# Kernel optimization log

Hardware: AMD Instinct MI355X
Metric: run time of the kernel (lower is better)

Reference implementation:

```python
import jax, jax.numpy as jnp
import numpy as np

WIDTH = 2048
NUM_HEADS = 16
HEAD_DIM = WIDTH // NUM_HEADS  # 128
ROPE_DIMS = HEAD_DIM // 2      # 64, partial rotary
WINDOW = 512
ROPE_BASE = 10000.0
NEG_INF = -1e9


def apply_rope(x, dims, offset=0, base=ROPE_BASE):
    # x: [B, H, L, hd]; non-traditional (half-split) rotary on first `dims` dims.
    L = x.shape[2]
    half = dims // 2
    pos = (offset + jnp.arange(L)).astype(x.dtype)                     # [L]
    inv_freq = jnp.exp(-jnp.log(jnp.asarray(base, x.dtype)) * (jnp.arange(0, dims, 2).astype(x.dtype) / dims))  # [half]
    theta = pos[:, None] * inv_freq[None, :]                           # [L, half]
    cos = jnp.cos(theta)[None, None]                                   # [1,1,L,half]
    sin = jnp.sin(theta)[None, None]
    x1 = x[..., :half]
    x2 = x[..., half:dims]
    rest = x[..., dims:]
    rx1 = x1 * cos - x2 * sin
    rx2 = x1 * sin + x2 * cos
    return jnp.concatenate([rx1, rx2, rest], axis=-1)


def setup_inputs() -> dict:
    key = jax.random.key(0)
    ks = jax.random.split(key, 6)
    B, L, D, hd = 2, 2048, WIDTH, HEAD_DIM
    x = jax.random.normal(ks[0], (B, L, D), dtype=jnp.float32)
    Wq = jax.random.normal(ks[1], (D, D), dtype=jnp.float32) * 0.02
    Wk = jax.random.normal(ks[2], (D, hd), dtype=jnp.float32) * 0.02
    Wv = jax.random.normal(ks[3], (D, hd), dtype=jnp.float32) * 0.02
    Wo = jax.random.normal(ks[4], (D, D), dtype=jnp.float32) * 0.02
    bo = jax.random.normal(ks[5], (D,), dtype=jnp.float32) * 0.02
    return {"x": x, "Wq": Wq, "Wk": Wk, "Wv": Wv, "Wo": Wo, "bo": bo}


def reference(x, Wq, Wk, Wv, Wo, bo):
    B, L, D = x.shape
    H, hd = NUM_HEADS, HEAD_DIM
    scale = hd ** (-0.5)

    q = (x @ Wq).reshape(B, L, H, hd).transpose(0, 2, 1, 3)   # [B,H,L,hd]
    k = (x @ Wk).reshape(B, L, 1, hd).transpose(0, 2, 1, 3)   # [B,1,L,hd] (MQA)
    v = (x @ Wv).reshape(B, L, 1, hd).transpose(0, 2, 1, 3)

    q = apply_rope(q, ROPE_DIMS)
    k = apply_rope(k, ROPE_DIMS)

    # sliding-window causal mask: attend iff 0 <= i - j < WINDOW
    i = jnp.arange(L)[:, None]
    j = jnp.arange(L)[None, :]
    allowed = (i - j >= 0) & (i - j < WINDOW)                  # [L,L]
    mask = jnp.where(allowed, 0.0, NEG_INF).astype(x.dtype)

    scores = jnp.einsum("bhqd,bkd->bhqk", q, k[:, 0]) * scale  # [B,H,L,L]
    scores = scores + mask[None, None]
    attn = jax.nn.softmax(scores, axis=-1)
    out = jnp.einsum("bhqk,bkd->bhqd", attn, v[:, 0])          # [B,H,L,hd]
    out = out.transpose(0, 2, 1, 3).reshape(B, L, D)
    return out @ Wo + bo
```

## Files before the change

### kernel.cpp

```cpp
#include <hip/hip_runtime.h>
#include <hip/hip_bf16.h>
#include <stdint.h>


typedef float  f32x4  __attribute__((ext_vector_type(4)));
typedef __bf16 bf16x8 __attribute__((ext_vector_type(8)));

#define ASYNC_LD16(gp, lp)                                                     \
  __builtin_amdgcn_global_load_lds(                                            \
      (__attribute__((address_space(1))) void*)(gp),                           \
      (__attribute__((address_space(3))) void*)(lp), 16, 0, 0)

__global__ __launch_bounds__(256) void prep_all(
    const float* __restrict__ x, __hip_bfloat16* __restrict__ xb,
    const float* __restrict__ Wq, const float* __restrict__ Wk,
    const float* __restrict__ Wv, const float* __restrict__ Wo,
    __hip_bfloat16* __restrict__ wqkvT, __hip_bfloat16* __restrict__ woT) {
  __shared__ float t[32][33];
  int bid = blockIdx.x;
  if (bid < 8192) {
    const int i = bid * 256 + threadIdx.x;
    const float4 v = ((const float4*)x)[i];
    __align__(8) __hip_bfloat16 o[4] = {
        __float2bfloat16(v.x), __float2bfloat16(v.y),
        __float2bfloat16(v.z), __float2bfloat16(v.w)};
    *(uint2*)(xb + (size_t)i * 4) = *(uint2*)o;
    return;
  }
  bid -= 8192;
  const float* src;
  __hip_bfloat16* dst;
  int C, cb, rb;
  if (bid < 4096) {
    src = Wq; dst = wqkvT; C = 2048; cb = bid & 63; rb = bid >> 6;
  } else if (bid < 4352) {
    const int l = bid - 4096;
    src = Wk; dst = wqkvT + 2048ull * 2048; C = 128; cb = l & 3; rb = l >> 2;
  } else if (bid < 4608) {
    const int l = bid - 4352;
    src = Wv; dst = wqkvT + 2176ull * 2048; C = 128; cb = l & 3; rb = l >> 2;
  } else {
    const int l = bid - 4608;
    src = Wo; dst = woT; C = 2048; cb = l & 63; rb = l >> 6;
  }
  const int c0 = cb * 32, r0 = rb * 32;
  const int xx = threadIdx.x & 31, y = threadIdx.x >> 5;
#pragma unroll
  for (int i = 0; i < 32; i += 8)
    t[y + i][xx] = src[(size_t)(r0 + y + i) * C + c0 + xx];
  __syncthreads();
#pragma unroll
  for (int i = 0; i < 32; i += 8)
    dst[(size_t)(c0 + y + i) * 2048 + r0 + xx] = __float2bfloat16(t[xx][y + i]);
}

__device__ __forceinline__ void gemm_core64(const __bf16* __restrict__ A,
                                            const __bf16* __restrict__ BT,
                                            int K, __bf16* As, __bf16* Bs,
                                            f32x4 (&acc)[4][4]) {
  const int tid = threadIdx.x;
  const int wave = tid >> 6;
  const int lane = tid & 63;
  const int m0 = blockIdx.y * 128;
  const int n0 = blockIdx.x * 128;
  const int wm = (wave & 1) * 64;
  const int wn = (wave >> 1) * 64;
  const int ln = lane & 15;
  const int quad = lane >> 4;
  const int rdoff = (quad ^ ((ln >> 1) & 3)) * 8;

  size_t goff[4];
  int ldsoff[4];
#pragma unroll
  for (int i = 0; i < 4; i++) {
    const int cidx = (wave * 4 + i) * 64 + lane;
    const int p = cidx >> 9;
    const int pidx = cidx & 511;
    const int row = pidx >> 2;
    const int cc = pidx & 3;
    const int cg = cc ^ ((row >> 1) & 3);
    goff[i] = (size_t)row * K + p * 32 + cg * 8;
    ldsoff[i] = (wave * 4 + i) * 512;
  }
  const __bf16* Abase = A + (size_t)m0 * K;
  const __bf16* Bbase = BT + (size_t)n0 * K;

  for (int k0 = 0; k0 < K; k0 += 64) {
#pragma unroll
    for (int i = 0; i < 4; i++)
      ASYNC_LD16(Abase + k0 + goff[i], As + ldsoff[i]);
#pragma unroll
    for (int i = 0; i < 4; i++)
      ASYNC_LD16(Bbase + k0 + goff[i], Bs + ldsoff[i]);
    __syncthreads();
    bf16x8 af[4][2], bf[4][2];
#pragma unroll
    for (int i = 0; i < 4; i++)
#pragma unroll
      for (int p = 0; p < 2; p++)
        af[i][p] = *(const bf16x8*)&As[p * 4096 + (wm + i * 16 + ln) * 32 + rdoff];
#pragma unroll
    for (int j = 0; j < 4; j++)
#pragma unroll
      for (int p = 0; p < 2; p++)
        bf[j][p] = *(const bf16x8*)&Bs[p * 4096 + (wn + j * 16 + ln) * 32 + rdoff];
#pragma unroll
    for (int p = 0; p < 2; p++)
#pragma unroll
      for (int i = 0; i < 4; i++)
#pragma unroll
        for (int j = 0; j < 4; j++)
          acc[i][j] = __builtin_amdgcn_mfma_f32_16x16x32_bf16(af[i][p], bf[j][p],
                                                              acc[i][j], 0, 0, 0);
    __syncthreads();
  }
}

__global__ __launch_bounds__(256) void gemm_qkv(
    const __bf16* __restrict__ A, const __bf16* __restrict__ BT,
    __hip_bfloat16* __restrict__ qd, __hip_bfloat16* __restrict__ kd,
    __hip_bfloat16* __restrict__ vtd, int K) {
  __shared__ __align__(16) __bf16 As[128 * 64];
  __shared__ __align__(16) __bf16 Bs[128 * 64];
  f32x4 acc[4][4];
  const f32x4 zero = {0.f, 0.f, 0.f, 0.f};
#pragma unroll
  for (int i = 0; i < 4; i++)
#pragma unroll
    for (int j = 0; j < 4; j++) acc[i][j] = zero;
  gemm_core64(A, BT, K, As, Bs, acc);

  const int tid = threadIdx.x;
  const int wave = tid >> 6;
  const int lane = tid & 63;
  const int quad = lane >> 4;
  const int ln = lane & 15;
  const int m0 = blockIdx.y * 128;
  const int n0 = blockIdx.x * 128;
  const int wm = (wave & 1) * 64;
  const int wn = (wave >> 1) * 64;

  if (n0 == 2176) {
    const int bb = m0 >> 11;
    const int mloc = m0 & 2047;
#pragma unroll
    for (int i = 0; i < 4; i++) {
      const int rb = mloc + wm + i * 16 + quad * 4;
#pragma unroll
      for (int j = 0; j < 4; j++) {
        const int col = wn + j * 16 + ln;
        __align__(8) __hip_bfloat16 t4[4];
#pragma unroll
        for (int r = 0; r < 4; r++) t4[r] = __float2bfloat16(acc[i][j][r]);
        *(uint2*)(vtd + ((size_t)(bb * 128 + col)) * 2048 + rb) = *(uint2*)t4;
      }
    }
    return;
  }

  __hip_bfloat16* dst;
  int dstride, dcol;
  if (n0 < 2048) {
    dst = qd; dstride = 2048; dcol = n0;
  } else {
    dst = kd; dstride = 128; dcol = 0;
  }
  const bool dorope = (wn == 0);
  float invf0 = 0.f, invf1 = 0.f;
  if (dorope) {
    invf0 = expf(-0.28782313662425574f * (float)ln);
    invf1 = expf(-0.28782313662425574f * (float)(16 + ln));
  }

#pragma unroll
  for (int i = 0; i < 4; i++) {
#pragma unroll
    for (int r = 0; r < 4; r++) {
      const int row = m0 + wm + i * 16 + quad * 4 + r;
      float o0 = acc[i][0][r], o1 = acc[i][1][r];
      float o2 = acc[i][2][r], o3 = acc[i][3][r];
      if (dorope) {
        const float pos = (float)(row & 2047);
        float s0, c0, s1, c1;
        __sincosf(pos * invf0, &s0, &c0);
        __sincosf(pos * invf1, &s1, &c1);
        const float a0 = o0, b0 = o2, a1 = o1, b1 = o3;
        o0 = a0 * c0 - b0 * s0;
        o2 = a0 * s0 + b0 * c0;
        o1 = a1 * c1 - b1 * s1;
        o3 = a1 * s1 + b1 * c1;
      }
      __hip_bfloat16* rp = dst + (size_t)row * dstride + dcol + wn + ln;
      rp[0]  = __float2bfloat16(o0);
      rp[16] = __float2bfloat16(o1);
      rp[32] = __float2bfloat16(o2);
      rp[48] = __float2bfloat16(o3);
    }
  }
}

__global__ __launch_bounds__(256) void gemm_out(
    const __bf16* __restrict__ A, const __bf16* __restrict__ BT,
    float* __restrict__ C, const float* __restrict__ bias, int N, int K) {
  __shared__ __align__(16) __bf16 As[128 * 64];
  __shared__ __align__(16) __bf16 Bs[128 * 64];
  f32x4 acc[4][4];
  const f32x4 zero = {0.f, 0.f, 0.f, 0.f};
#pragma unroll
  for (int i = 0; i < 4; i++)
#pragma unroll
    for (int j = 0; j < 4; j++) acc[i][j] = zero;
  gemm_core64(A, BT, K, As, Bs, acc);

  const int tid = threadIdx.x;
  const int wave = tid >> 6;
  const int lane = tid & 63;
  const int m0 = blockIdx.y * 128;
  const int n0 = blockIdx.x * 128;
  const int wm = (wave & 1) * 64;
  const int wn = (wave >> 1) * 64;
  const int lrow = lane & 15;
#pragma unroll
  for (int j = 0; j < 4; j++) {
    const int col = n0 + wn + j * 16 + lrow;
    const float bv = bias[col];
#pragma unroll
    for (int i = 0; i < 4; i++) {
#pragma unroll
      for (int r = 0; r < 4; r++) {
        const int row = m0 + wm + i * 16 + (lane >> 4) * 4 + r;
        C[(size_t)row * N + col] = acc[i][j][r] + bv;
      }
    }
  }
}

__global__ __launch_bounds__(256) void attn_mfma(
    const __bf16* __restrict__ qb,
    const __bf16* __restrict__ kb,
    const __bf16* __restrict__ vtb,
    __hip_bfloat16* __restrict__ o)
{
  __shared__ __align__(16) __bf16 Ks[4][64 * 32];
  __shared__ __align__(16) __bf16 Vs[2][128 * 32];
  __shared__ __align__(16) __bf16 Ps[4][2][2][512];
  const int tid = threadIdx.x;
  const int wave = tid >> 6;
  const int lane = tid & 63;
  const int quad = lane >> 4;
  const int ln = lane & 15;
  const int bid = blockIdx.x;
  const int q0 = (bid & 15) * 128;
  const int h = (bid >> 4) & 15;
  const int b = bid >> 8;
  const int swr = (ln >> 1) & 3;
  const int rdoff = (quad ^ swr) * 8;

  bf16x8 qf[2][4];
#pragma unroll
  for (int g = 0; g < 2; g++) {
    const __bf16* qrow =
        qb + ((size_t)(b * 2048 + q0 + wave * 32 + g * 16 + ln)) * 2048 + h * 128;
#pragma unroll
    for (int ks = 0; ks < 4; ks++)
      qf[g][ks] = *(const bf16x8*)(qrow + ks * 32 + quad * 8);
  }

  f32x4 oacc[2][8];
  const f32x4 zero = {0.f, 0.f, 0.f, 0.f};
#pragma unroll
  for (int g = 0; g < 2; g++)
#pragma unroll
    for (int nb = 0; nb < 8; nb++) oacc[g][nb] = zero;
  float li[2][4] = {{0.f, 0.f, 0.f, 0.f}, {0.f, 0.f, 0.f, 0.f}};
  const float scale = 0.08838834764831845f;

  const __bf16* kbase = kb + (size_t)b * 2048 * 128;
  const __bf16* vbase = vtb + (size_t)b * 128 * 2048;

  const int tstart = (q0 >= 512) ? 0 : (512 - q0) / 64;
  for (int t = tstart; t < 10; ++t) {
    const int jt = q0 - 512 + 64 * t;
    __syncthreads();
    {
      const int key4 = lane >> 2, uu = lane & 3;
      const int sw = (key4 >> 1) & 3;
#pragma unroll
      for (int i = 0; i < 4; ++i) {
        const int c = wave * 4 + i;
        const int ks = c & 3, keybase = (c >> 2) * 16;
        ASYNC_LD16(kbase + (size_t)(jt + keybase + key4) * 128 + ks * 32 +
                       (uu ^ sw) * 8,
                   &Ks[ks][keybase * 32]);
      }
#pragma unroll
      for (int i = 0; i < 4; ++i) {
        const int c = wave * 4 + i;
        const int p = c & 1, dbase = (c >> 1) * 16;
        ASYNC_LD16(vbase + (size_t)(dbase + key4) * 2048 + jt + p * 32 +
                       (uu ^ sw) * 8,
                   &Vs[p][dbase * 32]);
      }
    }
    __syncthreads();

    f32x4 sacc[2][4];
#pragma unroll
    for (int g = 0; g < 2; g++)
#pragma unroll
      for (int j = 0; j < 4; j++) sacc[g][j] = zero;
#pragma unroll
    for (int j = 0; j < 4; j++)
#pragma unroll
      for (int ks = 0; ks < 4; ks++) {
        const bf16x8 kf = *(const bf16x8*)&Ks[ks][(j * 16 + ln) * 32 + rdoff];
#pragma unroll
        for (int g = 0; g < 2; g++)
          sacc[g][j] = __builtin_amdgcn_mfma_f32_16x16x32_bf16(qf[g][ks], kf,
                                                               sacc[g][j], 0, 0, 0);
      }

#pragma unroll
    for (int g = 0; g < 2; g++)
#pragma unroll
      for (int j = 0; j < 4; j++)
#pragma unroll
        for (int r = 0; r < 4; r++) {
          float v = sacc[g][j][r] * scale;
          const int d0 = (wave * 32 + g * 16 + quad * 4 + r) - (j * 16 + ln);
          if (t <= 1 && d0 >= (t << 6)) v = -1e30f;
          if (t >= 8 && d0 < ((t - 8) << 6)) v = -1e30f;
          v = fminf(v, 60.f);
          const float p = __expf(v);
          li[g][r] += p;
          const int ch = (j & 1) * 2 + (ln >> 3);
          const int swp = (quad * 2 + (r >> 1)) & 3;
          Ps[wave][g][j >> 1]
            [(quad * 4 + r) * 32 + (ch ^ swp) * 8 + (ln & 7)] = (__bf16)p;
        }

    const bf16x8 pf00 = *(const bf16x8*)&Ps[wave][0][0][ln * 32 + rdoff];
    const bf16x8 pf01 = *(const bf16x8*)&Ps[wave][0][1][ln * 32 + rdoff];
    const bf16x8 pf10 = *(const bf16x8*)&Ps[wave][1][0][ln * 32 + rdoff];
    const bf16x8 pf11 = *(const bf16x8*)&Ps[wave][1][1][ln * 32 + rdoff];
#pragma unroll
    for (int nb = 0; nb < 8; nb++) {
      const bf16x8 vf0 = *(const bf16x8*)&Vs[0][(nb * 16 + ln) * 32 + rdoff];
      const bf16x8 vf1 = *(const bf16x8*)&Vs[1][(nb * 16 + ln) * 32 + rdoff];
      oacc[0][nb] =
          __builtin_amdgcn_mfma_f32_16x16x32_bf16(pf00, vf0, oacc[0][nb], 0, 0, 0);
      oacc[0][nb] =
          __builtin_amdgcn_mfma_f32_16x16x32_bf16(pf01, vf1, oacc[0][nb], 0, 0, 0);
      oacc[1][nb] =
          __builtin_amdgcn_mfma_f32_16x16x32_bf16(pf10, vf0, oacc[1][nb], 0, 0, 0);
      oacc[1][nb] =
          __builtin_amdgcn_mfma_f32_16x16x32_bf16(pf11, vf1, oacc[1][nb], 0, 0, 0);
    }
  }

#pragma unroll
  for (int off = 1; off < 16; off <<= 1)
#pragma unroll
    for (int g = 0; g < 2; g++)
#pragma unroll
      for (int r = 0; r < 4; r++) li[g][r] += __shfl_xor(li[g][r], off);

#pragma unroll
  for (int g = 0; g < 2; g++) {
    __hip_bfloat16* obase =
        o + ((size_t)(b * 2048 + q0 + wave * 32 + g * 16 + quad * 4)) * 2048 +
        h * 128 + ln;
#pragma unroll
    for (int r = 0; r < 4; r++) {
      const float inv = 1.0f / li[g][r];
#pragma unroll
      for (int nb = 0; nb < 8; nb++)
        obase[(size_t)r * 2048 + nb * 16] = __float2bfloat16(oacc[g][nb][r] * inv);
    }
  }
}

extern "C" void kernel_launch(void* const* d_in, const int* in_sizes, int n_in,
                              void* d_out, int out_size, void* d_ws,
                              size_t ws_size, hipStream_t stream) {
  const float* x = (const float*)d_in[0];
  const float* Wq = (const float*)d_in[1];
  const float* Wk = (const float*)d_in[2];
  const float* Wv = (const float*)d_in[3];
  const float* Wo = (const float*)d_in[4];
  const float* bo = (const float*)d_in[5];
  float* out = (float*)d_out;

  char* w = (char*)d_ws;
  auto alloc = [&](size_t bytes) {
    void* p = (void*)w;
    w += (bytes + 255) & ~(size_t)255;
    return p;
  };
  __bf16* xb = (__bf16*)alloc(4096ull * 2048 * 2);
  __hip_bfloat16* wqkvT = (__hip_bfloat16*)alloc(2304ull * 2048 * 2);
  __hip_bfloat16* woT = (__hip_bfloat16*)alloc(2048ull * 2048 * 2);
  __hip_bfloat16* qbuf = (__hip_bfloat16*)alloc(4096ull * 2048 * 2);
  __hip_bfloat16* kbuf = (__hip_bfloat16*)alloc(4096ull * 128 * 2);
  __hip_bfloat16* vtb = (__hip_bfloat16*)alloc(4096ull * 128 * 2);
  __hip_bfloat16* attnb = (__hip_bfloat16*)xb;

  prep_all<<<16896, 256, 0, stream>>>(x, (__hip_bfloat16*)xb, Wq, Wk, Wv, Wo,
                                      wqkvT, woT);

  gemm_qkv<<<dim3(18, 32), 256, 0, stream>>>(xb, (const __bf16*)wqkvT, qbuf,
                                             kbuf, vtb, 2048);

  attn_mfma<<<512, 256, 0, stream>>>((const __bf16*)qbuf, (const __bf16*)kbuf,
                                     (const __bf16*)vtb, attnb);

  gemm_out<<<dim3(16, 32), 256, 0, stream>>>((const __bf16*)attnb,
                                             (const __bf16*)woT, out, bo, 2048,
                                             2048);
}
```

Before: 260.4 us.

## Pipeline GEMM k-loop with 4-stage async LDS ring buffer and XCD-aware block remap

```diff
diff --git a/kernel.cpp b/kernel.cpp
--- a/kernel.cpp
+++ b/kernel.cpp
@@ -54,89 +54,132 @@
     dst[(size_t)(c0 + y + i) * 2048 + r0 + xx] = __float2bfloat16(t[xx][y + i]);
 }
 
-__device__ __forceinline__ void gemm_core64(const __bf16* __restrict__ A,
-                                            const __bf16* __restrict__ BT,
-                                            int K, __bf16* As, __bf16* Bs,
-                                            f32x4 (&acc)[4][4]) {
+template <int VM>
+__device__ __forceinline__ void wait_vm() {
+  if constexpr (VM == 8)
+    asm volatile("s_waitcnt vmcnt(8)" ::: "memory");
+  else if constexpr (VM == 4)
+    asm volatile("s_waitcnt vmcnt(4)" ::: "memory");
+  else
+    asm volatile("s_waitcnt vmcnt(0)" ::: "memory");
+}
+
+__device__ __forceinline__ void stage_tile(const __bf16* __restrict__ Ab,
+                                           const __bf16* __restrict__ Bb,
+                                           int k0, __bf16* as_, __bf16* bs_,
+                                           const size_t* goff,
+                                           const int* ldso) {
+#pragma unroll
+  for (int i = 0; i < 2; i++) ASYNC_LD16(Ab + k0 + goff[i], as_ + ldso[i]);
+#pragma unroll
+  for (int i = 0; i < 2; i++) ASYNC_LD16(Bb + k0 + goff[i], bs_ + ldso[i]);
+}
+
+template <int VM>
+__device__ __forceinline__ void tile_body(
+    int t, int NT, const __bf16* __restrict__ Ab, const __bf16* __restrict__ Bb,
+    __bf16 (&As)[4][4096], __bf16 (&Bs)[4][4096], const size_t* goff,
+    const int* ldso, int wm, int wn, int ln, int rdoff, f32x4 (&acc)[4][4]) {
+  wait_vm<VM>();
+  __builtin_amdgcn_s_barrier();
+  const __bf16* as_ = As[t & 3];
+  const __bf16* bs_ = Bs[t & 3];
+  bf16x8 af[4], bfr[4];
+#pragma unroll
+  for (int i = 0; i < 4; i++)
+    af[i] = *(const bf16x8*)&as_[(wm + i * 16 + ln) * 32 + rdoff];
+#pragma unroll
+  for (int j = 0; j < 4; j++)
+    bfr[j] = *(const bf16x8*)&bs_[(wn + j * 16 + ln) * 32 + rdoff];
+  if (t + 3 < NT)
+    stage_tile(Ab, Bb, (t + 3) * 32, As[(t + 3) & 3], Bs[(t + 3) & 3], goff,
+               ldso);
+  __builtin_amdgcn_s_setprio(1);
+#pragma unroll
+  for (int i = 0; i < 4; i++)
+#pragma unroll
+    for (int j = 0; j < 4; j++)
+      acc[i][j] = __builtin_amdgcn_mfma_f32_16x16x32_bf16(af[i], bfr[j],
+                                                          acc[i][j], 0, 0, 0);
+  __builtin_amdgcn_s_setprio(0);
+  __builtin_amdgcn_sched_barrier(0);
+  __builtin_amdgcn_s_barrier();
+}
+
+__device__ __forceinline__ void gemm_core_pipe(const __bf16* __restrict__ A,
+                                               const __bf16* __restrict__ BT,
+                                               int K, int m0, int n0,
+                                               __bf16 (&As)[4][4096],
+                                               __bf16 (&Bs)[4][4096],
+                                               f32x4 (&acc)[4][4]) {
   const int tid = threadIdx.x;
   const int wave = tid >> 6;
   const int lane = tid & 63;
-  const int m0 = blockIdx.y * 128;
-  const int n0 = blockIdx.x * 128;
   const int wm = (wave & 1) * 64;
   const int wn = (wave >> 1) * 64;
   const int ln = lane & 15;
   const int quad = lane >> 4;
   const int rdoff = (quad ^ ((ln >> 1) & 3)) * 8;
 
-  size_t goff[4];
-  int ldsoff[4];
-#pragma unroll
-  for (int i = 0; i < 4; i++) {
-    const int cidx = (wave * 4 + i) * 64 + lane;
-    const int p = cidx >> 9;
-    const int pidx = cidx & 511;
-    const int row = pidx >> 2;
-    const int cc = pidx & 3;
+  size_t goff[2];
+  int ldso[2];
+#pragma unroll
+  for (int i = 0; i < 2; i++) {
+    const int cidx = (wave * 2 + i) * 64 + lane;
+    const int row = cidx >> 2;
+    const int cc = cidx & 3;
     const int cg = cc ^ ((row >> 1) & 3);
-    goff[i] = (size_t)row * K + p * 32 + cg * 8;
-    ldsoff[i] = (wave * 4 + i) * 512;
-  }
-  const __bf16* Abase = A + (size_t)m0 * K;
-  const __bf16* Bbase = BT + (size_t)n0 * K;
-
-  for (int k0 = 0; k0 < K; k0 += 64) {
-#pragma unroll
-    for (int i = 0; i < 4; i++)
-      ASYNC_LD16(Abase + k0 + goff[i], As + ldsoff[i]);
-#pragma unroll
-    for (int i = 0; i < 4; i++)
-      ASYNC_LD16(Bbase + k0 + goff[i], Bs + ldsoff[i]);
-    __syncthreads();
-    bf16x8 af[4][2], bf[4][2];
-#pragma unroll
-    for (int i = 0; i < 4; i++)
-#pragma unroll
-      for (int p = 0; p < 2; p++)
-        af[i][p] = *(const bf16x8*)&As[p * 4096 + (wm + i * 16 + ln) * 32 + rdoff];
-#pragma unroll
-    for (int j = 0; j < 4; j++)
-#pragma unroll
-      for (int p = 0; p < 2; p++)
-        bf[j][p] = *(const bf16x8*)&Bs[p * 4096 + (wn + j * 16 + ln) * 32 + rdoff];
-#pragma unroll
-    for (int p = 0; p < 2; p++)
-#pragma unroll
-      for (int i = 0; i < 4; i++)
-#pragma unroll
-        for (int j = 0; j < 4; j++)
-          acc[i][j] = __builtin_amdgcn_mfma_f32_16x16x32_bf16(af[i][p], bf[j][p],
-                                                              acc[i][j], 0, 0, 0);
-    __syncthreads();
-  }
+    goff[i] = (size_t)row * K + cg * 8;
+    ldso[i] = (wave * 2 + i) * 512;
+  }
+  const __bf16* Ab = A + (size_t)m0 * K;
+  const __bf16* Bb = BT + (size_t)n0 * K;
+  const int NT = K >> 5;
+
+  stage_tile(Ab, Bb, 0, As[0], Bs[0], goff, ldso);
+  stage_tile(Ab, Bb, 32, As[1], Bs[1], goff, ldso);
+  stage_tile(Ab, Bb, 64, As[2], Bs[2], goff, ldso);
+
+  int t = 0;
+  for (; t < NT - 2; ++t)
+    tile_body<8>(t, NT, Ab, Bb, As, Bs, goff, ldso, wm, wn, ln, rdoff, acc);
+  tile_body<4>(t, NT, Ab, Bb, As, Bs, goff, ldso, wm, wn, ln, rdoff, acc);
+  ++t;
+  tile_body<0>(t, NT, Ab, Bb, As, Bs, goff, ldso, wm, wn, ln, rdoff, acc);
+}
+
+__device__ __forceinline__ void xcd_remap(int& bx, int& by) {
+  const int nwg = gridDim.x * gridDim.y;
+  const int flat = blockIdx.y * gridDim.x + blockIdx.x;
+  const int cpx = nwg >> 3;
+  const int nid = (flat & 7) * cpx + (flat >> 3);
+  bx = nid % gridDim.x;
+  by = nid / gridDim.x;
 }
 
 __global__ __launch_bounds__(256) void gemm_qkv(
     const __bf16* __restrict__ A, const __bf16* __restrict__ BT,
     __hip_bfloat16* __restrict__ qd, __hip_bfloat16* __restrict__ kd,
     __hip_bfloat16* __restrict__ vtd, int K) {
-  __shared__ __align__(16) __bf16 As[128 * 64];
-  __shared__ __align__(16) __bf16 Bs[128 * 64];
+  __shared__ __align__(16) __bf16 As[4][4096];
+  __shared__ __align__(16) __bf16 Bs[4][4096];
+  int bx, by;
+  xcd_remap(bx, by);
+  const int m0 = by * 128;
+  const int n0 = bx * 128;
   f32x4 acc[4][4];
   const f32x4 zero = {0.f, 0.f, 0.f, 0.f};
 #pragma unroll
   for (int i = 0; i < 4; i++)
 #pragma unroll
     for (int j = 0; j < 4; j++) acc[i][j] = zero;
-  gemm_core64(A, BT, K, As, Bs, acc);
+  gemm_core_pipe(A, BT, K, m0, n0, As, Bs, acc);
 
   const int tid = threadIdx.x;
   const int wave = tid >> 6;
   const int lane = tid & 63;
   const int quad = lane >> 4;
   const int ln = lane & 15;
-  const int m0 = blockIdx.y * 128;
-  const int n0 = blockIdx.x * 128;
   const int wm = (wave & 1) * 64;
   const int wn = (wave >> 1) * 64;
 
@@ -202,21 +245,23 @@
 __global__ __launch_bounds__(256) void gemm_out(
     const __bf16* __restrict__ A, const __bf16* __restrict__ BT,
     float* __restrict__ C, const float* __restrict__ bias, int N, int K) {
-  __shared__ __align__(16) __bf16 As[128 * 64];
-  __shared__ __align__(16) __bf16 Bs[128 * 64];
+  __shared__ __align__(16) __bf16 As[4][4096];
+  __shared__ __align__(16) __bf16 Bs[4][4096];
+  int bx, by;
+  xcd_remap(bx, by);
+  const int m0 = by * 128;
+  const int n0 = bx * 128;
   f32x4 acc[4][4];
   const f32x4 zero = {0.f, 0.f, 0.f, 0.f};
 #pragma unroll
   for (int i = 0; i < 4; i++)
 #pragma unroll
     for (int j = 0; j < 4; j++) acc[i][j] = zero;
-  gemm_core64(A, BT, K, As, Bs, acc);
+  gemm_core_pipe(A, BT, K, m0, n0, As, Bs, acc);
 
   const int tid = threadIdx.x;
   const int wave = tid >> 6;
   const int lane = tid & 63;
-  const int m0 = blockIdx.y * 128;
-  const int n0 = blockIdx.x * 128;
   const int wm = (wave & 1) * 64;
   const int wn = (wave >> 1) * 64;
   const int lrow = lane & 15;
```

Result: slower. 271.3 us (+4.2%).

## Use 8-wave GEMM blocks and XCD-aware block remapping for projection GEMMs

Applied to the files above, without the earlier changes.

```diff
diff --git a/kernel.cpp b/kernel.cpp
--- a/kernel.cpp
+++ b/kernel.cpp
@@ -54,48 +54,55 @@
     dst[(size_t)(c0 + y + i) * 2048 + r0 + xx] = __float2bfloat16(t[xx][y + i]);
 }
 
+__device__ __forceinline__ void xcd_remap(int& bx, int& by) {
+  const int nwg = gridDim.x * gridDim.y;
+  const int flat = blockIdx.y * gridDim.x + blockIdx.x;
+  const int cpx = nwg >> 3;
+  const int nid = (flat & 7) * cpx + (flat >> 3);
+  bx = nid % gridDim.x;
+  by = nid / gridDim.x;
+}
+
 __device__ __forceinline__ void gemm_core64(const __bf16* __restrict__ A,
                                             const __bf16* __restrict__ BT,
-                                            int K, __bf16* As, __bf16* Bs,
-                                            f32x4 (&acc)[4][4]) {
+                                            int K, int m0, int n0, __bf16* As,
+                                            __bf16* Bs, f32x4 (&acc)[2][4]) {
   const int tid = threadIdx.x;
   const int wave = tid >> 6;
   const int lane = tid & 63;
-  const int m0 = blockIdx.y * 128;
-  const int n0 = blockIdx.x * 128;
-  const int wm = (wave & 1) * 64;
-  const int wn = (wave >> 1) * 64;
+  const int wm = (wave & 3) * 32;
+  const int wn = (wave >> 2) * 64;
   const int ln = lane & 15;
   const int quad = lane >> 4;
   const int rdoff = (quad ^ ((ln >> 1) & 3)) * 8;
 
-  size_t goff[4];
-  int ldsoff[4];
-#pragma unroll
-  for (int i = 0; i < 4; i++) {
-    const int cidx = (wave * 4 + i) * 64 + lane;
+  size_t goff[2];
+  int ldsoff[2];
+#pragma unroll
+  for (int i = 0; i < 2; i++) {
+    const int cidx = (wave * 2 + i) * 64 + lane;
     const int p = cidx >> 9;
     const int pidx = cidx & 511;
     const int row = pidx >> 2;
     const int cc = pidx & 3;
     const int cg = cc ^ ((row >> 1) & 3);
     goff[i] = (size_t)row * K + p * 32 + cg * 8;
-    ldsoff[i] = (wave * 4 + i) * 512;
+    ldsoff[i] = (wave * 2 + i) * 512;
   }
   const __bf16* Abase = A + (size_t)m0 * K;
   const __bf16* Bbase = BT + (size_t)n0 * K;
 
   for (int k0 = 0; k0 < K; k0 += 64) {
 #pragma unroll
-    for (int i = 0; i < 4; i++)
+    for (int i = 0; i < 2; i++)
       ASYNC_LD16(Abase + k0 + goff[i], As + ldsoff[i]);
 #pragma unroll
-    for (int i = 0; i < 4; i++)
+    for (int i = 0; i < 2; i++)
       ASYNC_LD16(Bbase + k0 + goff[i], Bs + ldsoff[i]);
     __syncthreads();
-    bf16x8 af[4][2], bf[4][2];
-#pragma unroll
-    for (int i = 0; i < 4; i++)
+    bf16x8 af[2][2], bf[4][2];
+#pragma unroll
+    for (int i = 0; i < 2; i++)
 #pragma unroll
       for (int p = 0; p < 2; p++)
         af[i][p] = *(const bf16x8*)&As[p * 4096 + (wm + i * 16 + ln) * 32 + rdoff];
@@ -107,7 +114,7 @@
 #pragma unroll
     for (int p = 0; p < 2; p++)
 #pragma unroll
-      for (int i = 0; i < 4; i++)
+      for (int i = 0; i < 2; i++)
 #pragma unroll
         for (int j = 0; j < 4; j++)
           acc[i][j] = __builtin_amdgcn_mfma_f32_16x16x32_bf16(af[i][p], bf[j][p],
@@ -116,35 +123,37 @@
   }
 }
 
-__global__ __launch_bounds__(256) void gemm_qkv(
+__global__ __launch_bounds__(512) void gemm_qkv(
     const __bf16* __restrict__ A, const __bf16* __restrict__ BT,
     __hip_bfloat16* __restrict__ qd, __hip_bfloat16* __restrict__ kd,
     __hip_bfloat16* __restrict__ vtd, int K) {
   __shared__ __align__(16) __bf16 As[128 * 64];
   __shared__ __align__(16) __bf16 Bs[128 * 64];
-  f32x4 acc[4][4];
+  int bx, by;
+  xcd_remap(bx, by);
+  const int m0 = by * 128;
+  const int n0 = bx * 128;
+  f32x4 acc[2][4];
   const f32x4 zero = {0.f, 0.f, 0.f, 0.f};
 #pragma unroll
-  for (int i = 0; i < 4; i++)
+  for (int i = 0; i < 2; i++)
 #pragma unroll
     for (int j = 0; j < 4; j++) acc[i][j] = zero;
-  gemm_core64(A, BT, K, As, Bs, acc);
+  gemm_core64(A, BT, K, m0, n0, As, Bs, acc);
 
   const int tid = threadIdx.x;
   const int wave = tid >> 6;
   const int lane = tid & 63;
   const int quad = lane >> 4;
   const int ln = lane & 15;
-  const int m0 = blockIdx.y * 128;
-  const int n0 = blockIdx.x * 128;
-  const int wm = (wave & 1) * 64;
-  const int wn = (wave >> 1) * 64;
+  const int wm = (wave & 3) * 32;
+  const int wn = (wave >> 2) * 64;
 
   if (n0 == 2176) {
     const int bb = m0 >> 11;
     const int mloc = m0 & 2047;
 #pragma unroll
-    for (int i = 0; i < 4; i++) {
+    for (int i = 0; i < 2; i++) {
       const int rb = mloc + wm + i * 16 + quad * 4;
 #pragma unroll
       for (int j = 0; j < 4; j++) {
@@ -173,7 +182,7 @@
   }
 
 #pragma unroll
-  for (int i = 0; i < 4; i++) {
+  for (int i = 0; i < 2; i++) {
 #pragma unroll
     for (int r = 0; r < 4; r++) {
       const int row = m0 + wm + i * 16 + quad * 4 + r;
@@ -199,33 +208,35 @@
   }
 }
 
-__global__ __launch_bounds__(256) void gemm_out(
+__global__ __launch_bounds__(512) void gemm_out(
     const __bf16* __restrict__ A, const __bf16* __restrict__ BT,
     float* __restrict__ C, const float* __restrict__ bias, int N, int K) {
   __shared__ __align__(16) __bf16 As[128 * 64];
   __shared__ __align__(16) __bf16 Bs[128 * 64];
-  f32x4 acc[4][4];
+  int bx, by;
+  xcd_remap(bx, by);
+  const int m0 = by * 128;
+  const int n0 = bx * 128;
+  f32x4 acc[2][4];
   const f32x4 zero = {0.f, 0.f, 0.f, 0.f};
 #pragma unroll
-  for (int i = 0; i < 4; i++)
+  for (int i = 0; i < 2; i++)
 #pragma unroll
     for (int j = 0; j < 4; j++) acc[i][j] = zero;
-  gemm_core64(A, BT, K, As, Bs, acc);
+  gemm_core64(A, BT, K, m0, n0, As, Bs, acc);
 
   const int tid = threadIdx.x;
   const int wave = tid >> 6;
   const int lane = tid & 63;
-  const int m0 = blockIdx.y * 128;
-  const int n0 = blockIdx.x * 128;
-  const int wm = (wave & 1) * 64;
-  const int wn = (wave >> 1) * 64;
+  const int wm = (wave & 3) * 32;
+  const int wn = (wave >> 2) * 64;
   const int lrow = lane & 15;
 #pragma unroll
   for (int j = 0; j < 4; j++) {
     const int col = n0 + wn + j * 16 + lrow;
     const float bv = bias[col];
 #pragma unroll
-    for (int i = 0; i < 4; i++) {
+    for (int i = 0; i < 2; i++) {
 #pragma unroll
       for (int r = 0; r < 4; r++) {
         const int row = m0 + wm + i * 16 + (lane >> 4) * 4 + r;
@@ -408,13 +419,13 @@
   prep_all<<<16896, 256, 0, stream>>>(x, (__hip_bfloat16*)xb, Wq, Wk, Wv, Wo,
                                       wqkvT, woT);
 
-  gemm_qkv<<<dim3(18, 32), 256, 0, stream>>>(xb, (const __bf16*)wqkvT, qbuf,
+  gemm_qkv<<<dim3(18, 32), 512, 0, stream>>>(xb, (const __bf16*)wqkvT, qbuf,
                                              kbuf, vtb, 2048);
 
   attn_mfma<<<512, 256, 0, stream>>>((const __bf16*)qbuf, (const __bf16*)kbuf,
                                      (const __bf16*)vtb, attnb);
 
-  gemm_out<<<dim3(16, 32), 256, 0, stream>>>((const __bf16*)attnb,
+  gemm_out<<<dim3(16, 32), 512, 0, stream>>>((const __bf16*)attnb,
                                              (const __bf16*)woT, out, bo, 2048,
                                              2048);
 }
```

Measured after the change: 264.3 us. No clear change (+1.5%).
